# Performance work log

Measured on AMD Instinct MI355X. Metric: run time of the kernel, lower is better.

Reference implementation:

```python
import jax, jax.numpy as jnp
import numpy as np

LARGE_NUMBER = 1.0e10
B, NV, H = 512, 48, 32


def setup_inputs() -> dict:
    key = jax.random.key(0)
    k_z, k_wc, k_bc, k_wy, k_by, k_m = jax.random.split(key, 6)
    z = jax.random.normal(k_z, (B * NV, H), dtype=jnp.float32)
    Wc = jax.random.normal(k_wc, (H, H), dtype=jnp.float32) * 0.05
    bc = jax.random.normal(k_bc, (H,), dtype=jnp.float32) * 0.05
    Wy = jax.random.normal(k_wy, (H, H), dtype=jnp.float32) * 0.05
    by = jax.random.normal(k_by, (H,), dtype=jnp.float32) * 0.05
    mask = (jax.random.uniform(k_m, (B * NV, 1)) > 0.3).astype(jnp.int32)
    return {"z": z, "Wc": Wc, "bc": bc, "Wy": Wy, "by": by,
            "mask": mask, "num_graphs": B, "nv": NV}


def reference(z, Wc, bc, Wy, by, mask, num_graphs, nv):
    # Faithful translation of Attention.forward (sigmoid-gated pairwise node attention).
    # torch.nn.Linear(x) == x @ W.T + b; applying Linear after tiling == tiling after Linear.
    h = Wc.shape[0]
    m = mask.reshape(num_graphs, nv, 1).astype(z.dtype)            # (B, nv, 1)
    zc = (z @ Wc.T + bc).reshape(num_graphs, nv, h)                 # lin_attention_c
    zy = (z @ Wy.T + by).reshape(num_graphs, nv, h)                 # lin_attention_y
    # atten_mask_c + atten_mask_yi = (m_i + m_j)*L - 2L, broadcast over H
    mask_add = (m[:, :, None, :] + m[:, None, :, :]) * LARGE_NUMBER - 2.0 * LARGE_NUMBER
    s = jax.nn.sigmoid(zc[:, :, None, :] + zy[:, None, :, :] + mask_add)  # (B, nv, nv, H)
    denom = jnp.sum(m, axis=1, keepdims=True)                       # (B, 1, 1) valid-node count
    atten_mi = jnp.sum(s, axis=2) / denom                           # (B, nv, H)
    return atten_mi.reshape(-1, h)
```

## Files before the change

### kernel.cpp

```cpp
#include <hip/hip_runtime.h>


#define LOG2E 1.4426950408889634f

typedef float v2f __attribute__((ext_vector_type(2)));

constexpr int NV = 48;
constexpr int H  = 32;
constexpr int BLOCK = 768;
constexpr int WPAD = 36;
constexpr float F_INV = 1.0e8f;

__global__ __launch_bounds__(BLOCK, 6)
void OptLinker_attn_kernel(const float* __restrict__ z,
                           const float* __restrict__ Wc,
                           const float* __restrict__ bc,
                           const float* __restrict__ Wy,
                           const float* __restrict__ by,
                           const int*   __restrict__ mask,
                           float* __restrict__ out)
{
    __shared__ float z_s[NV * H];
    __shared__ float F_s[NV * H];
    __shared__ float wc_s[H * WPAD];
    __shared__ float wy_s[H * WPAD];

    const int b   = blockIdx.x;
    const int tid = threadIdx.x;
    const int h   = tid & 31;
    const int i0  = tid >> 5;

    const int lane = tid & 63;
    const int mv = (lane < NV) ? mask[b * NV + lane] : 0;
    const float bcv = bc[h], byv = by[h];

    const float4* zb4 = (const float4*)(z + (size_t)b * (NV * H));
    if (tid < (NV * H) / 4) ((float4*)z_s)[tid] = zb4[tid];

    if (tid < 512) {
        const int q = tid & 255;
        const float4 v = (tid < 256) ? ((const float4*)Wc)[q]
                                     : ((const float4*)Wy)[q];
        float* dst = (tid < 256 ? wc_s : wy_s) + (q >> 3) * WPAD + (q & 7) * 4;
        *(float4*)dst = v;
    }

    const unsigned long long bits = __ballot(mv != 0);

    __syncthreads();

    const int r0 = i0, r1 = i0 + 24;
    const float4* zr0 = (const float4*)(z_s + r0 * H);
    const float4* zr1 = (const float4*)(z_s + r1 * H);

    float E0, E1;
    {
        float4 w[8];
        const float* wr = wc_s + h * WPAD;
        #pragma unroll
        for (int q = 0; q < 8; ++q) w[q] = *(const float4*)(wr + q * 4);
        v2f a0 = {0.f, 0.f}, a1 = {0.f, 0.f};
        #pragma unroll
        for (int q = 0; q < 8; ++q) {
            const float4 z0 = zr0[q], z1 = zr1[q];
            const v2f wlo = {w[q].x, w[q].y}, whi = {w[q].z, w[q].w};
            a0 = __builtin_elementwise_fma((v2f){z0.x, z0.y}, wlo, a0);
            a0 = __builtin_elementwise_fma((v2f){z0.z, z0.w}, whi, a0);
            a1 = __builtin_elementwise_fma((v2f){z1.x, z1.y}, wlo, a1);
            a1 = __builtin_elementwise_fma((v2f){z1.z, z1.w}, whi, a1);
        }
        E0 = __builtin_amdgcn_exp2f(-(a0.x + a0.y + bcv) * LOG2E);
        E1 = __builtin_amdgcn_exp2f(-(a1.x + a1.y + bcv) * LOG2E);
    }

    {
        float4 w[8];
        const float* wr = wy_s + h * WPAD;
        #pragma unroll
        for (int q = 0; q < 8; ++q) w[q] = *(const float4*)(wr + q * 4);
        v2f a0 = {0.f, 0.f}, a1 = {0.f, 0.f};
        #pragma unroll
        for (int q = 0; q < 8; ++q) {
            const float4 z0 = zr0[q], z1 = zr1[q];
            const v2f wlo = {w[q].x, w[q].y}, whi = {w[q].z, w[q].w};
            a0 = __builtin_elementwise_fma((v2f){z0.x, z0.y}, wlo, a0);
            a0 = __builtin_elementwise_fma((v2f){z0.z, z0.w}, whi, a0);
            a1 = __builtin_elementwise_fma((v2f){z1.x, z1.y}, wlo, a1);
            a1 = __builtin_elementwise_fma((v2f){z1.z, z1.w}, whi, a1);
        }
        F_s[r0 * H + h] = ((bits >> r0) & 1ull)
            ? __builtin_amdgcn_exp2f(-(a0.x + a0.y + byv) * LOG2E) : F_INV;
        F_s[r1 * H + h] = ((bits >> r1) & 1ull)
            ? __builtin_amdgcn_exp2f(-(a1.x + a1.y + byv) * LOG2E) : F_INV;
    }

    __syncthreads();

    const v2f E2  = {E0, E1};
    const v2f one = {1.f, 1.f};
    v2f acc2 = {0.f, 0.f};
    #pragma unroll
    for (int j = 0; j < NV; j += 4) {
        const float f0 = F_s[(j + 0) * H + h];
        const float f1 = F_s[(j + 1) * H + h];
        const float f2 = F_s[(j + 2) * H + h];
        const float f3 = F_s[(j + 3) * H + h];
        const v2f t0 = __builtin_elementwise_fma(E2, (v2f){f0, f0}, one);
        const v2f t1 = __builtin_elementwise_fma(E2, (v2f){f1, f1}, one);
        const v2f t2 = __builtin_elementwise_fma(E2, (v2f){f2, f2}, one);
        const v2f t3 = __builtin_elementwise_fma(E2, (v2f){f3, f3}, one);
        const v2f p01 = t0 * t1, p23 = t2 * t3;
        const v2f num = __builtin_elementwise_fma(t0 + t1, p23, (t2 + t3) * p01);
        const v2f den = p01 * p23;
        v2f r;
        r.x = __builtin_amdgcn_rcpf(den.x);
        r.y = __builtin_amdgcn_rcpf(den.y);
        acc2 = __builtin_elementwise_fma(num, r, acc2);
    }

    const int nvalid = __popcll(bits);
    const float rden = __builtin_amdgcn_rcpf((float)nvalid);
    float* ob = out + (size_t)b * (NV * H);
    ob[r0 * H + h] = ((bits >> r0) & 1ull) ? acc2.x * rden : 0.0f;
    ob[r1 * H + h] = ((bits >> r1) & 1ull) ? acc2.y * rden : 0.0f;
}

extern "C" void kernel_launch(void* const* d_in, const int* in_sizes, int n_in,
                              void* d_out, int out_size, void* d_ws, size_t ws_size,
                              hipStream_t stream) {
    const float* z    = (const float*)d_in[0];
    const float* Wc   = (const float*)d_in[1];
    const float* bc   = (const float*)d_in[2];
    const float* Wy   = (const float*)d_in[3];
    const float* by   = (const float*)d_in[4];
    const int*   mask = (const int*)d_in[5];
    float* out = (float*)d_out;

    const int ngraph = in_sizes[0] / (NV * H);
    OptLinker_attn_kernel<<<ngraph, BLOCK, 0, stream>>>(z, Wc, bc, Wy, by, mask, out);
}
```

Before: 11.27 us.

## Read z directly from global and transpose F into padded shared layout

Drops the shared-memory staging of z, so each thread reads its two z rows straight from global memory (relying on cache broadcast across the 32 h-lanes). F is now stored transposed with a padded stride of 52, so the inner j-loop reads four F values with a single float4 LDS load instead of four scalar loads. This cuts LDS traffic and shared-memory footprint, but global z loads are now issued twice (once per projection) and may cost more latency than the LDS path, and the transposed F stores may see bank conflicts.

Result: slower. 11.56 us (+2.6%).

```diff
diff --git a/kernel.cpp b/kernel.cpp
--- a/kernel.cpp
+++ b/kernel.cpp
@@ -9,6 +9,7 @@
 constexpr int H  = 32;
 constexpr int BLOCK = 768;
 constexpr int WPAD = 36;
+constexpr int FSTRIDE = 52;
 constexpr float F_INV = 1.0e8f;
 
 __global__ __launch_bounds__(BLOCK, 6)
@@ -20,22 +21,19 @@
                            const int*   __restrict__ mask,
                            float* __restrict__ out)
 {
-    __shared__ float z_s[NV * H];
-    __shared__ float F_s[NV * H];
     __shared__ float wc_s[H * WPAD];
     __shared__ float wy_s[H * WPAD];
+    __shared__ float F_t[H * FSTRIDE];
 
     const int b   = blockIdx.x;
     const int tid = threadIdx.x;
     const int h   = tid & 31;
     const int i0  = tid >> 5;
+    const int r0  = i0, r1 = i0 + 24;
+    const int lane = tid & 63;
 
-    const int lane = tid & 63;
     const int mv = (lane < NV) ? mask[b * NV + lane] : 0;
     const float bcv = bc[h], byv = by[h];
-
-    const float4* zb4 = (const float4*)(z + (size_t)b * (NV * H));
-    if (tid < (NV * H) / 4) ((float4*)z_s)[tid] = zb4[tid];
 
     if (tid < 512) {
         const int q = tid & 255;
@@ -47,11 +45,10 @@
 
     const unsigned long long bits = __ballot(mv != 0);
 
+    const float4* zr0 = (const float4*)(z + (size_t)b * (NV * H) + r0 * H);
+    const float4* zr1 = (const float4*)(z + (size_t)b * (NV * H) + r1 * H);
+
     __syncthreads();
-
-    const int r0 = i0, r1 = i0 + 24;
-    const float4* zr0 = (const float4*)(z_s + r0 * H);
-    const float4* zr1 = (const float4*)(z_s + r1 * H);
 
     float E0, E1;
     {
@@ -62,12 +59,12 @@
         v2f a0 = {0.f, 0.f}, a1 = {0.f, 0.f};
         #pragma unroll
         for (int q = 0; q < 8; ++q) {
-            const float4 z0 = zr0[q], z1 = zr1[q];
+            const float4 x0 = zr0[q], x1 = zr1[q];
             const v2f wlo = {w[q].x, w[q].y}, whi = {w[q].z, w[q].w};
-            a0 = __builtin_elementwise_fma((v2f){z0.x, z0.y}, wlo, a0);
-            a0 = __builtin_elementwise_fma((v2f){z0.z, z0.w}, whi, a0);
-            a1 = __builtin_elementwise_fma((v2f){z1.x, z1.y}, wlo, a1);
-            a1 = __builtin_elementwise_fma((v2f){z1.z, z1.w}, whi, a1);
+            a0 = __builtin_elementwise_fma((v2f){x0.x, x0.y}, wlo, a0);
+            a0 = __builtin_elementwise_fma((v2f){x0.z, x0.w}, whi, a0);
+            a1 = __builtin_elementwise_fma((v2f){x1.x, x1.y}, wlo, a1);
+            a1 = __builtin_elementwise_fma((v2f){x1.z, x1.w}, whi, a1);
         }
         E0 = __builtin_amdgcn_exp2f(-(a0.x + a0.y + bcv) * LOG2E);
         E1 = __builtin_amdgcn_exp2f(-(a1.x + a1.y + bcv) * LOG2E);
@@ -81,16 +78,16 @@
         v2f a0 = {0.f, 0.f}, a1 = {0.f, 0.f};
         #pragma unroll
         for (int q = 0; q < 8; ++q) {
-            const float4 z0 = zr0[q], z1 = zr1[q];
+            const float4 x0 = zr0[q], x1 = zr1[q];
             const v2f wlo = {w[q].x, w[q].y}, whi = {w[q].z, w[q].w};
-            a0 = __builtin_elementwise_fma((v2f){z0.x, z0.y}, wlo, a0);
-            a0 = __builtin_elementwise_fma((v2f){z0.z, z0.w}, whi, a0);
-            a1 = __builtin_elementwise_fma((v2f){z1.x, z1.y}, wlo, a1);
-            a1 = __builtin_elementwise_fma((v2f){z1.z, z1.w}, whi, a1);
+            a0 = __builtin_elementwise_fma((v2f){x0.x, x0.y}, wlo, a0);
+            a0 = __builtin_elementwise_fma((v2f){x0.z, x0.w}, whi, a0);
+            a1 = __builtin_elementwise_fma((v2f){x1.x, x1.y}, wlo, a1);
+            a1 = __builtin_elementwise_fma((v2f){x1.z, x1.w}, whi, a1);
         }
-        F_s[r0 * H + h] = ((bits >> r0) & 1ull)
+        F_t[h * FSTRIDE + r0] = ((bits >> r0) & 1ull)
             ? __builtin_amdgcn_exp2f(-(a0.x + a0.y + byv) * LOG2E) : F_INV;
-        F_s[r1 * H + h] = ((bits >> r1) & 1ull)
+        F_t[h * FSTRIDE + r1] = ((bits >> r1) & 1ull)
             ? __builtin_amdgcn_exp2f(-(a1.x + a1.y + byv) * LOG2E) : F_INV;
     }
 
@@ -99,16 +96,14 @@
     const v2f E2  = {E0, E1};
     const v2f one = {1.f, 1.f};
     v2f acc2 = {0.f, 0.f};
+    const float4* frow = (const float4*)(F_t + h * FSTRIDE);
     #pragma unroll
-    for (int j = 0; j < NV; j += 4) {
-        const float f0 = F_s[(j + 0) * H + h];
-        const float f1 = F_s[(j + 1) * H + h];
-        const float f2 = F_s[(j + 2) * H + h];
-        const float f3 = F_s[(j + 3) * H + h];
-        const v2f t0 = __builtin_elementwise_fma(E2, (v2f){f0, f0}, one);
-        const v2f t1 = __builtin_elementwise_fma(E2, (v2f){f1, f1}, one);
-        const v2f t2 = __builtin_elementwise_fma(E2, (v2f){f2, f2}, one);
-        const v2f t3 = __builtin_elementwise_fma(E2, (v2f){f3, f3}, one);
+    for (int jq = 0; jq < NV / 4; ++jq) {
+        const float4 f = frow[jq];
+        const v2f t0 = __builtin_elementwise_fma(E2, (v2f){f.x, f.x}, one);
+        const v2f t1 = __builtin_elementwise_fma(E2, (v2f){f.y, f.y}, one);
+        const v2f t2 = __builtin_elementwise_fma(E2, (v2f){f.z, f.z}, one);
+        const v2f t3 = __builtin_elementwise_fma(E2, (v2f){f.w, f.w}, one);
         const v2f p01 = t0 * t1, p23 = t2 * t3;
         const v2f num = __builtin_elementwise_fma(t0 + t1, p23, (t2 + t3) * p01);
         const v2f den = p01 * p23;
```
